# Kernel tuning notes

Measured on AMD Instinct MI355X. Metric: run time of the kernel, lower is better.

## Reference

```python
import jax, jax.numpy as jnp
from jax import lax
import numpy as np

B, S, H, L, NH, DH, DFF, V, NL = 8, 512, 768, 12, 12, 64, 3072, 30522, 19


def _ln(x, s, b):
    m = x.mean(-1, keepdims=True)
    v = ((x - m) ** 2).mean(-1, keepdims=True)
    return (x - m) * lax.rsqrt(v + 1e-12) * s + b


def setup_inputs() -> dict:
    key = jax.random.key(0)
    ks = iter(jax.random.split(key, 40))

    def n(shape, scale=0.02):
        return jax.random.normal(next(ks), shape, jnp.float32) * scale

    return {
        "input_ids": jax.random.randint(next(ks), (B, S), 0, V, jnp.int32),
        "attention_mask": jnp.ones((B, S), jnp.int32),
        "labels": jax.random.randint(next(ks), (B, S), 0, NL, jnp.int32),
        "token_emb": n((V, H)), "pos_emb": n((S, H)),
        "ln_emb_s": jnp.ones((H,)), "ln_emb_b": jnp.zeros((H,)),
        "Wq": n((L, H, H)), "bq": jnp.zeros((L, H)),
        "Wk": n((L, H, H)), "bk": jnp.zeros((L, H)),
        "Wv": n((L, H, H)), "bv": jnp.zeros((L, H)),
        "Wo": n((L, H, H)), "bo": jnp.zeros((L, H)),
        "ln1_s": jnp.ones((L, H)), "ln1_b": jnp.zeros((L, H)),
        "W1": n((L, H, DFF)), "b1": jnp.zeros((L, DFF)),
        "W2": n((L, DFF, H)), "b2": jnp.zeros((L, H)),
        "ln2_s": jnp.ones((L, H)), "ln2_b": jnp.zeros((L, H)),
        "cls_W": n((H, NL)), "cls_b": jnp.zeros((NL,)),
        "start_trans": n((NL,), 0.1), "end_trans": n((NL,), 0.1),
        "trans": n((NL, NL), 0.1),
    }


def reference(input_ids, attention_mask, labels, token_emb, pos_emb, ln_emb_s, ln_emb_b,
              Wq, bq, Wk, bk, Wv, bv, Wo, bo, ln1_s, ln1_b, W1, b1, W2, b2,
              ln2_s, ln2_b, cls_W, cls_b, start_trans, end_trans, trans):
    maskf = attention_mask.astype(jnp.float32)
    # --- BERT encoder (post-LN, eval mode so dropout is identity) ---
    x = token_emb[input_ids] + pos_emb[None, :, :]
    x = _ln(x, ln_emb_s, ln_emb_b)
    bias = (1.0 - maskf)[:, None, None, :] * -1e9  # additive attention mask
    scale = 1.0 / np.sqrt(DH)
    for l in range(L):
        q = (x @ Wq[l] + bq[l]).reshape(B, S, NH, DH)
        k = (x @ Wk[l] + bk[l]).reshape(B, S, NH, DH)
        v = (x @ Wv[l] + bv[l]).reshape(B, S, NH, DH)
        a = jax.nn.softmax(jnp.einsum('bqhd,bkhd->bhqk', q, k) * scale + bias, -1)
        ctx = jnp.einsum('bhqk,bkhd->bqhd', a, v).reshape(B, S, H)
        x = _ln(x + ctx @ Wo[l] + bo[l], ln1_s[l], ln1_b[l])
        h = jax.nn.gelu(x @ W1[l] + b1[l])
        x = _ln(x + h @ W2[l] + b2[l], ln2_s[l], ln2_b[l])
    logits = x @ cls_W + cls_b  # [B, S, NL]
    # --- CRF negative log-likelihood (torchcrf semantics, reduction='sum') ---
    em = jnp.take_along_axis(logits, labels[..., None], -1)[..., 0]  # [B, S]
    num = start_trans[labels[:, 0]] + em[:, 0]
    tr = trans[labels[:, :-1], labels[:, 1:]]  # [B, S-1]
    num = num + jnp.sum((tr + em[:, 1:]) * maskf[:, 1:], -1)
    last_idx = maskf.sum(-1).astype(jnp.int32) - 1
    last_tag = jnp.take_along_axis(labels, last_idx[:, None], 1)[:, 0]
    num = num + end_trans[last_tag]
    # forward algorithm (log-domain DP scan over time)
    alpha0 = start_trans[None, :] + logits[:, 0]  # [B, NL]

    def step(alpha, inp):
        em_t, m_t = inp  # [B, NL], [B]
        nxt = jax.nn.logsumexp(alpha[:, :, None] + trans[None] + em_t[:, None, :], axis=1)
        return jnp.where(m_t[:, None] > 0, nxt, alpha), None

    alpha, _ = lax.scan(step, alpha0,
                        (jnp.swapaxes(logits, 0, 1)[1:], jnp.swapaxes(maskf, 0, 1)[1:]))
    den = jax.nn.logsumexp(alpha + end_trans[None, :], -1)
    return jnp.sum(den - num)  # loss = -sum(llh)
```

## Files before the change

### kernel.cpp

```cpp
#include <hip/hip_runtime.h>
#include <hip/hip_bf16.h>
#include <math.h>

#define B_   8
#define S_   512
#define H_   768
#define L_   12
#define NHD_ 12
#define DH_  64
#define DFF_ 3072
#define NL_  19

#define NCH_ 32
#define CHL_ 16

typedef __bf16 bf16x8 __attribute__((ext_vector_type(8)));
typedef float  f32x4  __attribute__((ext_vector_type(4)));

__device__ __forceinline__ unsigned short f2bf(float f) {
    unsigned int u = __float_as_uint(f);
    u = (u + 0x7fffu + ((u >> 16) & 1u)) >> 16;
    return (unsigned short)u;
}

__device__ __forceinline__ float gelu_f(float x) {
    const float c = 0.7978845608028654f;
    float x3 = x * x * x;
    return 0.5f * x * (1.0f + tanhf(c * (x + 0.044715f * x3)));
}

__device__ __forceinline__ void load_lds16(const unsigned short* g, unsigned short* l) {
    __builtin_amdgcn_global_load_lds(
        (const __attribute__((address_space(1))) unsigned int*)g,
        (__attribute__((address_space(3))) unsigned int*)l,
        16, 0, 0);
}

__global__ __launch_bounds__(256) void prep_layer(
    const float* __restrict__ Wq, const float* __restrict__ Wk,
    const float* __restrict__ Wv, const float* __restrict__ Wo,
    const float* __restrict__ W1, const float* __restrict__ W2,
    const float* __restrict__ bq, const float* __restrict__ bk,
    const float* __restrict__ bv,
    unsigned short* __restrict__ WqkvT, unsigned short* __restrict__ WoT,
    unsigned short* __restrict__ W1T, unsigned short* __restrict__ W2T,
    float* __restrict__ biasc)
{
    __shared__ float t[64][65];
    const int tid = threadIdx.x;
    const int id = blockIdx.x;

    if (id >= 1728) {
        int i = (id - 1728) * 256 + tid;
        if (i < 3 * H_) biasc[i] = (i < H_) ? bq[i] : (i < 2 * H_ ? bk[i - H_] : bv[i - 2 * H_]);
        return;
    }

    const float* src; unsigned short* dst; int K, N, bx, by;
    if (id < 576) {
        int wsel = id / 144, tt = id % 144;
        bx = tt % 12; by = tt / 12; K = H_; N = H_;
        src = (wsel == 0) ? Wq : (wsel == 1) ? Wk : (wsel == 2) ? Wv : Wo;
        dst = (wsel < 3) ? (WqkvT + (size_t)wsel * H_ * H_) : WoT;
    } else if (id < 1152) {
        int tt = id - 576; bx = tt % 48; by = tt / 48; K = H_; N = DFF_; src = W1; dst = W1T;
    } else {
        int tt = id - 1152; bx = tt % 12; by = tt / 12; K = DFF_; N = H_; src = W2; dst = W2T;
    }

    const int n0 = bx * 64, k0 = by * 64;
    #pragma unroll
    for (int p = 0; p < 16; ++p) {
        int idx = p * 256 + tid;
        int i = idx >> 6, j = idx & 63;
        t[i][j] = src[(size_t)(k0 + i) * N + n0 + j];
    }
    __syncthreads();
    #pragma unroll
    for (int p = 0; p < 4; ++p) {
        int q = p * 256 + tid;
        int n = q >> 4, kq = q & 15;
        unsigned int w0 = (unsigned int)f2bf(t[kq * 4 + 0][n]) | ((unsigned int)f2bf(t[kq * 4 + 1][n]) << 16);
        unsigned int w1 = (unsigned int)f2bf(t[kq * 4 + 2][n]) | ((unsigned int)f2bf(t[kq * 4 + 3][n]) << 16);
        uint2 w; w.x = w0; w.y = w1;
        *(uint2*)(dst + (size_t)(n0 + n) * K + k0 + kq * 4) = w;
    }
}

template <int EPI>
__global__ __launch_bounds__(256) void gemm_bf16(
    const unsigned short* __restrict__ A,
    const unsigned short* __restrict__ Bt,
    const float* __restrict__ bias,
    const float* __restrict__ R,
    float* __restrict__ Cf,
    unsigned short* __restrict__ Cb,
    unsigned short* __restrict__ Vt,
    int M, int N, int K)
{
    __shared__ __align__(16) unsigned short As[128 * 32];
    __shared__ __align__(16) unsigned short Bs[128 * 32];
    const int tid  = threadIdx.x;
    const int lane = tid & 63;
    const int wave = tid >> 6;
    const int wm = wave >> 1, wn = wave & 1;
    const int mbase = blockIdx.y * 128;
    const int nbase = blockIdx.x * 128;

    f32x4 acc[4][4];
    #pragma unroll
    for (int mi = 0; mi < 4; ++mi)
        #pragma unroll
        for (int ni = 0; ni < 4; ++ni) acc[mi][ni] = (f32x4){0.f, 0.f, 0.f, 0.f};

    const int crow = tid >> 2;
    const int kc   = tid & 3;
    const unsigned short* ag0 = A  + (size_t)(mbase + crow) * K + kc * 8;
    const unsigned short* ag1 = A  + (size_t)(mbase + 64 + crow) * K + kc * 8;
    const unsigned short* bg0 = Bt + (size_t)(nbase + crow) * K + kc * 8;
    const unsigned short* bg1 = Bt + (size_t)(nbase + 64 + crow) * K + kc * 8;
    unsigned short* la0 = As + (size_t)tid * 8;
    unsigned short* la1 = As + (size_t)(256 + tid) * 8;
    unsigned short* lb0 = Bs + (size_t)tid * 8;
    unsigned short* lb1 = Bs + (size_t)(256 + tid) * 8;

    const int fr = lane & 15;
    const int fc = lane >> 4;

    for (int kk = 0; kk < K; kk += 32) {
        load_lds16(ag0 + kk, la0);
        load_lds16(ag1 + kk, la1);
        load_lds16(bg0 + kk, lb0);
        load_lds16(bg1 + kk, lb1);
        __syncthreads();

        bf16x8 af[4], bf[4];
        #pragma unroll
        for (int mi = 0; mi < 4; ++mi)
            af[mi] = *(const bf16x8*)&As[(size_t)(wm * 64 + mi * 16 + fr) * 32 + fc * 8];
        #pragma unroll
        for (int ni = 0; ni < 4; ++ni)
            bf[ni] = *(const bf16x8*)&Bs[(size_t)(wn * 64 + ni * 16 + fr) * 32 + fc * 8];

        #pragma unroll
        for (int mi = 0; mi < 4; ++mi)
            #pragma unroll
            for (int ni = 0; ni < 4; ++ni)
                acc[mi][ni] = __builtin_amdgcn_mfma_f32_16x16x32_bf16(
                    af[mi], bf[ni], acc[mi][ni], 0, 0, 0);
        __syncthreads();
    }

    const int r0 = (lane >> 4) * 4;
    const int c0 = lane & 15;
    #pragma unroll
    for (int mi = 0; mi < 4; ++mi) {
        const int gm = mbase + wm * 64 + mi * 16 + r0;
        #pragma unroll
        for (int ni = 0; ni < 4; ++ni) {
            const int gn = nbase + wn * 64 + ni * 16 + c0;
            const float bv = bias[gn];
            #pragma unroll
            for (int r = 0; r < 4; ++r) {
                float vv = acc[mi][ni][r] + bv;
                const size_t off = (size_t)(gm + r) * N + gn;
                if (EPI == 1) Cb[off] = f2bf(gelu_f(vv));
                else if (EPI == 2) Cf[off] = vv + R[off];
                else {
                    unsigned short v16 = f2bf(vv);
                    if (gn < 2 * H_) {
                        Cb[off] = v16;
                    } else {
                        int tok = gm + r;
                        Vt[(((size_t)(tok >> 9) * NHD_ + ((gn - 2 * H_) >> 6)) * DH_
                            + (gn & 63)) * S_ + (tok & (S_ - 1))] = v16;
                    }
                }
            }
        }
    }
}

__global__ __launch_bounds__(256) void attn3(
    const unsigned short* __restrict__ qkvb,
    const unsigned short* __restrict__ vtb,
    const int* __restrict__ mask,
    unsigned short* __restrict__ ctxb)
{
    const int qt = blockIdx.x, h = blockIdx.y, b = blockIdx.z;
    const int tid = threadIdx.x;
    const int lane = tid & 63;
    const int w  = tid >> 6;
    const int fr = lane & 15;
    const int fh = lane >> 4;
    const int bh = b * NHD_ + h;

    __shared__ __align__(16) unsigned short Ks[64 * 64];
    __shared__ __align__(16) unsigned short Vts[64 * 64];
    __shared__ __align__(16) unsigned short Ps[4][16][72];
    __shared__ float Ms[64];

    const size_t qrow = (size_t)((b << 9) + (qt << 6) + (w << 4) + fr) * 2304 + (h << 6);
    const bf16x8 qf0 = *(const bf16x8*)&qkvb[qrow + fh * 8];
    const bf16x8 qf1 = *(const bf16x8*)&qkvb[qrow + 32 + fh * 8];

    float m = -1e30f, l = 0.f;
    f32x4 po[4];
    #pragma unroll
    for (int dg = 0; dg < 4; ++dg) po[dg] = (f32x4){0.f, 0.f, 0.f, 0.f};

    const int swz = (fr & 7) << 4;

    for (int kt = 0; kt < 8; ++kt) {
        const int kb = kt << 6;
        __syncthreads();
        {
            int i0 = tid, i1 = tid + 256;
            int r0s = i0 >> 3, r1s = i1 >> 3;
            int c0 = ((i0 & 7) << 4) ^ ((r0s & 7) << 4);
            int c1 = ((i1 & 7) << 4) ^ ((r1s & 7) << 4);
            load_lds16(qkvb + (size_t)((b << 9) + kb + r0s) * 2304 + H_ + (h << 6) + (c0 >> 1), Ks + i0 * 8);
            load_lds16(qkvb + (size_t)((b << 9) + kb + r1s) * 2304 + H_ + (h << 6) + (c1 >> 1), Ks + i1 * 8);
            load_lds16(vtb + ((size_t)(bh << 6) + r0s) * S_ + kb + (c0 >> 1), Vts + i0 * 8);
            load_lds16(vtb + ((size_t)(bh << 6) + r1s) * S_ + kb + (c1 >> 1), Vts + i1 * 8);
        }
        if (tid < 64) Ms[tid] = (1.0f - (float)mask[(b << 9) + kb + tid]) * -1e9f;
        __syncthreads();

        f32x4 sc4[4];
        #pragma unroll
        for (int g = 0; g < 4; ++g) sc4[g] = (f32x4){0.f, 0.f, 0.f, 0.f};
        #pragma unroll
        for (int c = 0; c < 2; ++c) {
            const bf16x8 qf = c ? qf1 : qf0;
            #pragma unroll
            for (int g = 0; g < 4; ++g) {
                bf16x8 kf = *(const bf16x8*)&Ks[((g << 4) + fr) * 64
                              + ((((c << 6) + (fh << 4)) ^ swz) >> 1)];
                sc4[g] = __builtin_amdgcn_mfma_f32_16x16x32_bf16(kf, qf, sc4[g], 0, 0, 0);
            }
        }

        float sv[16];
        float pm = -3e38f;
        #pragma unroll
        for (int g = 0; g < 4; ++g)
            #pragma unroll
            for (int r = 0; r < 4; ++r) {
                float xx = sc4[g][r] * 0.125f + Ms[(g << 4) + (fh << 2) + r];
                sv[g * 4 + r] = xx;
                pm = fmaxf(pm, xx);
            }
        pm = fmaxf(pm, __shfl_xor(pm, 16));
        pm = fmaxf(pm, __shfl_xor(pm, 32));
        const float mnew = fmaxf(m, pm);
        const float alpha = __expf(m - mnew);
        float ps = 0.f;
        #pragma unroll
        for (int i = 0; i < 16; ++i) { sv[i] = __expf(sv[i] - mnew); ps += sv[i]; }
        ps += __shfl_xor(ps, 16);
        ps += __shfl_xor(ps, 32);
        l = l * alpha + ps;
        m = mnew;

        #pragma unroll
        for (int g = 0; g < 4; ++g) {
            unsigned int* pw = (unsigned int*)&Ps[w][fr][(g << 4) + (fh << 2)];
            pw[0] = (unsigned int)f2bf(sv[g * 4 + 0]) | ((unsigned int)f2bf(sv[g * 4 + 1]) << 16);
            pw[1] = (unsigned int)f2bf(sv[g * 4 + 2]) | ((unsigned int)f2bf(sv[g * 4 + 3]) << 16);
        }

        float al[4];
        #pragma unroll
        for (int r = 0; r < 4; ++r) al[r] = __shfl(alpha, (fh << 2) + r);
        #pragma unroll
        for (int dg = 0; dg < 4; ++dg) {
            po[dg][0] *= al[0]; po[dg][1] *= al[1];
            po[dg][2] *= al[2]; po[dg][3] *= al[3];
        }

        const bf16x8 pf0 = *(const bf16x8*)&Ps[w][fr][fh * 8];
        const bf16x8 pf1 = *(const bf16x8*)&Ps[w][fr][32 + fh * 8];
        #pragma unroll
        for (int dg = 0; dg < 4; ++dg) {
            bf16x8 vf0 = *(const bf16x8*)&Vts[((dg << 4) + fr) * 64 + (((fh << 4) ^ swz) >> 1)];
            po[dg] = __builtin_amdgcn_mfma_f32_16x16x32_bf16(pf0, vf0, po[dg], 0, 0, 0);
            bf16x8 vf1 = *(const bf16x8*)&Vts[((dg << 4) + fr) * 64 + (((64 + (fh << 4)) ^ swz) >> 1)];
            po[dg] = __builtin_amdgcn_mfma_f32_16x16x32_bf16(pf1, vf1, po[dg], 0, 0, 0);
        }
    }

    float inv[4];
    #pragma unroll
    for (int r = 0; r < 4; ++r) inv[r] = 1.0f / __shfl(l, (fh << 2) + r);
    #pragma unroll
    for (int r = 0; r < 4; ++r) {
        unsigned short* op = ctxb
            + (size_t)((b << 9) + (qt << 6) + (w << 4) + (fh << 2) + r) * H_
            + (h << 6) + fr;
        #pragma unroll
        for (int dg = 0; dg < 4; ++dg)
            op[dg << 4] = f2bf(po[dg][r] * inv[r]);
    }
}

__global__ __launch_bounds__(256) void ln_kernel(
    const float* __restrict__ in, const float* __restrict__ sc,
    const float* __restrict__ bi, float* __restrict__ out,
    unsigned short* __restrict__ outb)
{
    const int row = blockIdx.x;
    const int tid = threadIdx.x;
    const float* x = in + (size_t)row * H_;
    float v[3], s0 = 0.f, s1 = 0.f;
    #pragma unroll
    for (int r = 0; r < 3; ++r) {
        v[r] = x[tid + r * 256];
        s0 += v[r]; s1 += v[r] * v[r];
    }
    __shared__ float red[8];
    __shared__ float stat[2];
    #pragma unroll
    for (int o = 32; o > 0; o >>= 1) { s0 += __shfl_down(s0, o); s1 += __shfl_down(s1, o); }
    if ((tid & 63) == 0) { red[tid >> 6] = s0; red[4 + (tid >> 6)] = s1; }
    __syncthreads();
    if (tid == 0) {
        float t0 = red[0] + red[1] + red[2] + red[3];
        float t1 = red[4] + red[5] + red[6] + red[7];
        float mean = t0 / H_;
        float var  = t1 / H_ - mean * mean;
        stat[0] = mean;
        stat[1] = rsqrtf(var + 1e-12f);
    }
    __syncthreads();
    float mean = stat[0], rstd = stat[1];
    float* o = out + (size_t)row * H_;
    unsigned short* ob = outb + (size_t)row * H_;
    #pragma unroll
    for (int r = 0; r < 3; ++r) {
        int i = tid + r * 256;
        float rr = (v[r] - mean) * rstd * sc[i] + bi[i];
        o[i] = rr;
        ob[i] = f2bf(rr);
    }
}

__global__ __launch_bounds__(256) void embed_ln_kernel(
    const int* __restrict__ ids, const float* __restrict__ tok,
    const float* __restrict__ pos, const float* __restrict__ sc,
    const float* __restrict__ bi, float* __restrict__ out,
    unsigned short* __restrict__ outb)
{
    const int row = blockIdx.x;
    const int spos = row & (S_ - 1);
    const int tid = threadIdx.x;
    const int id = ids[row];
    const float* t = tok + (size_t)id * H_;
    const float* p = pos + (size_t)spos * H_;
    float v[3], s0 = 0.f, s1 = 0.f;
    #pragma unroll
    for (int r = 0; r < 3; ++r) {
        int i = tid + r * 256;
        v[r] = t[i] + p[i];
        s0 += v[r]; s1 += v[r] * v[r];
    }
    __shared__ float red[8];
    __shared__ float stat[2];
    #pragma unroll
    for (int o = 32; o > 0; o >>= 1) { s0 += __shfl_down(s0, o); s1 += __shfl_down(s1, o); }
    if ((tid & 63) == 0) { red[tid >> 6] = s0; red[4 + (tid >> 6)] = s1; }
    __syncthreads();
    if (tid == 0) {
        float t0 = red[0] + red[1] + red[2] + red[3];
        float t1 = red[4] + red[5] + red[6] + red[7];
        float mean = t0 / H_;
        float var  = t1 / H_ - mean * mean;
        stat[0] = mean;
        stat[1] = rsqrtf(var + 1e-12f);
    }
    __syncthreads();
    float mean = stat[0], rstd = stat[1];
    float* o = out + (size_t)row * H_;
    unsigned short* ob = outb + (size_t)row * H_;
    #pragma unroll
    for (int r = 0; r < 3; ++r) {
        int i = tid + r * 256;
        float rr = (v[r] - mean) * rstd * sc[i] + bi[i];
        o[i] = rr;
        ob[i] = f2bf(rr);
    }
}

__global__ __launch_bounds__(256) void gemm_cls(
    const float* __restrict__ A, const float* __restrict__ W,
    const float* __restrict__ bias, float* __restrict__ C, int M, int N, int K)
{
    __shared__ float As[16][65];
    __shared__ float Ws[16][64];
    const int tid = threadIdx.x;
    const int tx = tid & 15;
    const int ty = tid >> 4;
    const int mbase = blockIdx.y * 64;
    const int nbase = blockIdx.x * 64;
    float acc[4][4] = {};
    for (int kk = 0; kk < K; kk += 16) {
        #pragma unroll
        for (int r = 0; r < 4; ++r) {
            int idx = r * 256 + tid;
            int mm = idx >> 4, k4 = idx & 15;
            As[k4][mm] = A[(size_t)(mbase + mm) * K + kk + k4];
        }
        #pragma unroll
        for (int r = 0; r < 4; ++r) {
            int idx = r * 256 + tid;
            int n = idx & 63, k4 = idx >> 6;
            int gn = nbase + n;
            Ws[k4][n] = (gn < N) ? W[(size_t)(kk + k4) * N + gn] : 0.0f;
        }
        __syncthreads();
        #pragma unroll
        for (int k = 0; k < 16; ++k) {
            float a[4], w[4];
            #pragma unroll
            for (int i = 0; i < 4; ++i) a[i] = As[k][ty * 4 + i];
            #pragma unroll
            for (int j = 0; j < 4; ++j) w[j] = Ws[k][tx * 4 + j];
            #pragma unroll
            for (int i = 0; i < 4; ++i)
                #pragma unroll
                for (int j = 0; j < 4; ++j)
                    acc[i][j] = fmaf(a[i], w[j], acc[i][j]);
        }
        __syncthreads();
    }
    #pragma unroll
    for (int i = 0; i < 4; ++i) {
        int gm = mbase + ty * 4 + i;
        #pragma unroll
        for (int j = 0; j < 4; ++j) {
            int gn = nbase + tx * 4 + j;
            if (gn < N) C[(size_t)gm * N + gn] = acc[i][j] + bias[gn];
        }
    }
}

__global__ __launch_bounds__(256) void crf_num_kernel(
    const float* __restrict__ logits, const int* __restrict__ labels,
    const int* __restrict__ mask, const float* __restrict__ start_trans,
    const float* __restrict__ end_trans, const float* __restrict__ trans,
    float* __restrict__ numb)
{
    const int b = blockIdx.x;
    const int tid = threadIdx.x;
    float lsum = 0.f, lmask = 0.f;
    for (int t = tid; t < S_; t += 256) {
        float mf = (float)mask[b * S_ + t];
        lmask += mf;
        if (t >= 1) {
            int lp = labels[b * S_ + t - 1];
            int lc = labels[b * S_ + t];
            float em = logits[((size_t)b * S_ + t) * NL_ + lc];
            lsum += (trans[lp * NL_ + lc] + em) * mf;
        }
    }
    __shared__ float red[8];
    #pragma unroll
    for (int o = 32; o > 0; o >>= 1) { lsum += __shfl_down(lsum, o); lmask += __shfl_down(lmask, o); }
    if ((tid & 63) == 0) { red[tid >> 6] = lsum; red[4 + (tid >> 6)] = lmask; }
    __syncthreads();
    if (tid == 0) {
        float ts = red[0] + red[1] + red[2] + red[3];
        float tm = red[4] + red[5] + red[6] + red[7];
        int l0 = labels[b * S_];
        float nm = start_trans[l0] + logits[(size_t)b * S_ * NL_ + l0] + ts;
        int last = (int)tm - 1;
        int lt = labels[b * S_ + last];
        nm += end_trans[lt];
        numb[b] = nm;
    }
}

__global__ __launch_bounds__(384) void crf_chunk_kernel(
    const float* __restrict__ logits, const int* __restrict__ mask,
    const float* __restrict__ trans, float* __restrict__ Pg)
{
    const int c = blockIdx.x, b = blockIdx.y;
    const int tid = threadIdx.x;
    const bool act = tid < NL_ * NL_;
    const int i = tid / NL_;
    const int j = tid - i * NL_;

    const int t0 = 1 + c * CHL_;
    const int nt = min(CHL_, S_ - t0);

    __shared__ float P[NL_][20];
    __shared__ float tr_s[NL_ * NL_];
    __shared__ float em_s[CHL_ * NL_];
    __shared__ int mk[CHL_];

    for (int f = tid; f < NL_ * NL_; f += 384) tr_s[f] = trans[f];
    for (int f = tid; f < nt * NL_; f += 384)
        em_s[f] = logits[((size_t)b * S_ + t0) * NL_ + f];
    if (tid < nt) mk[tid] = mask[b * S_ + t0 + tid];
    __syncthreads();

    float trcol[NL_];
    if (act) {
        #pragma unroll
        for (int k = 0; k < NL_; ++k) trcol[k] = tr_s[k * NL_ + j];
        float p0;
        if (mk[0] > 0) p0 = tr_s[i * NL_ + j] + em_s[j];
        else           p0 = (i == j) ? 0.f : -1e30f;
        P[i][j] = p0;
    }
    __syncthreads();

    for (int tt = 1; tt < nt; ++tt) {
        float nv = 0.f;
        if (act) {
            float v[NL_];
            float vmax = -3e38f;
            #pragma unroll
            for (int k = 0; k < NL_; ++k) {
                v[k] = P[i][k] + trcol[k];
                vmax = fmaxf(vmax, v[k]);
            }
            float s = 0.f;
            #pragma unroll
            for (int k = 0; k < NL_; ++k) s += __expf(v[k] - vmax);
            nv = vmax + __logf(s) + em_s[tt * NL_ + j];
        }
        __syncthreads();
        if (act && mk[tt] > 0) P[i][j] = nv;
        __syncthreads();
    }

    if (act) Pg[((size_t)b * NCH_ + c) * (NL_ * NL_) + tid] = P[i][j];
}

__global__ __launch_bounds__(384) void crf_combine_kernel(
    const float* __restrict__ Pg, const float* __restrict__ logits,
    const float* __restrict__ start_trans, const float* __restrict__ end_trans,
    float* __restrict__ denb)
{
    const int b = blockIdx.x;
    const int tid = threadIdx.x;
    __shared__ float Q[NCH_ * NL_ * NL_];
    __shared__ float fin[NL_];

    for (int w = tid; w < NCH_ * NL_ * NL_; w += 384)
        Q[w] = Pg[(size_t)b * NCH_ * NL_ * NL_ + w];
    __syncthreads();

    for (int m = NCH_ / 2; m >= 1; m >>= 1) {
        const int items = m * NL_ * NL_;
        float res[16];
        #pragma unroll
        for (int r = 0; r < 16; ++r) {
            const int w = tid + r * 384;
            if (w < items) {
                const int p = w / (NL_ * NL_);
                const int e = w - p * (NL_ * NL_);
                const int ii = e / NL_;
                const int jj = e - ii * NL_;
                const float* Lm = &Q[(2 * p) * NL_ * NL_ + ii * NL_];
                const float* Rm = &Q[(2 * p + 1) * NL_ * NL_ + jj];
                float v[NL_];
                float vmax = -3e38f;
                #pragma unroll
                for (int k = 0; k < NL_; ++k) {
                    v[k] = Lm[k] + Rm[k * NL_];
                    vmax = fmaxf(vmax, v[k]);
                }
                float s = 0.f;
                #pragma unroll
                for (int k = 0; k < NL_; ++k) s += __expf(v[k] - vmax);
                res[r] = vmax + __logf(s);
            }
        }
        __syncthreads();
        #pragma unroll
        for (int r = 0; r < 16; ++r) {
            const int w = tid + r * 384;
            if (w < items) Q[w] = res[r];
        }
        __syncthreads();
    }

    if (tid < NL_) {
        float v[NL_];
        float vmax = -3e38f;
        #pragma unroll
        for (int k = 0; k < NL_; ++k) {
            v[k] = start_trans[k] + logits[(size_t)b * S_ * NL_ + k] + Q[k * NL_ + tid];
            vmax = fmaxf(vmax, v[k]);
        }
        float s = 0.f;
        #pragma unroll
        for (int k = 0; k < NL_; ++k) s += __expf(v[k] - vmax);
        fin[tid] = vmax + __logf(s) + end_trans[tid];
    }
    __syncthreads();
    if (tid == 0) {
        float vmax = -3e38f;
        #pragma unroll
        for (int k = 0; k < NL_; ++k) vmax = fmaxf(vmax, fin[k]);
        float s = 0.f;
        #pragma unroll
        for (int k = 0; k < NL_; ++k) s += __expf(fin[k] - vmax);
        denb[b] = vmax + __logf(s);
    }
}

__global__ void finalize_kernel(const float* __restrict__ numb,
                                const float* __restrict__ denb,
                                float* __restrict__ out)
{
    if (threadIdx.x == 0 && blockIdx.x == 0) {
        float s = 0.f;
        for (int b = 0; b < B_; ++b) s += denb[b] - numb[b];
        out[0] = s;
    }
}

extern "C" void kernel_launch(void* const* d_in, const int* in_sizes, int n_in,
                              void* d_out, int out_size, void* d_ws, size_t ws_size,
                              hipStream_t stream)
{
    const int*   input_ids = (const int*)d_in[0];
    const int*   attn_mask = (const int*)d_in[1];
    const int*   labels    = (const int*)d_in[2];
    const float* token_emb = (const float*)d_in[3];
    const float* pos_emb   = (const float*)d_in[4];
    const float* ln_emb_s  = (const float*)d_in[5];
    const float* ln_emb_b  = (const float*)d_in[6];
    const float* Wq  = (const float*)d_in[7];
    const float* bq  = (const float*)d_in[8];
    const float* Wk  = (const float*)d_in[9];
    const float* bk  = (const float*)d_in[10];
    const float* Wv  = (const float*)d_in[11];
    const float* bv  = (const float*)d_in[12];
    const float* Wo  = (const float*)d_in[13];
    const float* bo  = (const float*)d_in[14];
    const float* ln1s = (const float*)d_in[15];
    const float* ln1b = (const float*)d_in[16];
    const float* W1  = (const float*)d_in[17];
    const float* b1  = (const float*)d_in[18];
    const float* W2  = (const float*)d_in[19];
    const float* b2  = (const float*)d_in[20];
    const float* ln2s = (const float*)d_in[21];
    const float* ln2b = (const float*)d_in[22];
    const float* cls_W = (const float*)d_in[23];
    const float* cls_b = (const float*)d_in[24];
    const float* start_trans = (const float*)d_in[25];
    const float* end_trans   = (const float*)d_in[26];
    const float* trans       = (const float*)d_in[27];

    char* base = (char*)d_ws;
    const int M = B_ * S_;
    unsigned short* qkvb = (unsigned short*)base;
    unsigned short* vtb  = qkvb + (size_t)M * 2304;
    unsigned short* hbb  = (unsigned short*)base;
    size_t off = (size_t)M * 3072 * 2;
    float*          x     = (float*)(base + off); off += (size_t)M * H_ * 4;
    float*          y     = (float*)(base + off); off += (size_t)M * H_ * 4;
    unsigned short* xb    = (unsigned short*)(base + off); off += (size_t)M * H_ * 2;
    unsigned short* ctxb  = (unsigned short*)(base + off); off += (size_t)M * H_ * 2;
    unsigned short* WqkvT = (unsigned short*)(base + off); off += (size_t)3 * H_ * H_ * 2;
    unsigned short* WoT   = (unsigned short*)(base + off); off += (size_t)H_ * H_ * 2;
    unsigned short* W1T   = (unsigned short*)(base + off); off += (size_t)DFF_ * H_ * 2;
    unsigned short* W2T   = (unsigned short*)(base + off); off += (size_t)H_ * DFF_ * 2;
    float*          biasc = (float*)(base + off); off += 3 * H_ * 4 + 256;
    float*          logits= (float*)(base + off); off += (size_t)M * NL_ * 4;
    float*          numb  = (float*)(base + off); off += 32;
    float*          denb  = (float*)(base + off); off += 32;
    float*          Pg    = (float*)(base + off); off += (size_t)B_ * NCH_ * NL_ * NL_ * 4;

    dim3 blk(256);
    embed_ln_kernel<<<M, blk, 0, stream>>>(input_ids, token_emb, pos_emb, ln_emb_s, ln_emb_b, x, xb);

    for (int l = 0; l < L_; ++l) {
        const size_t oHH = (size_t)l * H_ * H_;
        const size_t oHF = (size_t)l * H_ * DFF_;
        prep_layer<<<1737, blk, 0, stream>>>(
            Wq + oHH, Wk + oHH, Wv + oHH, Wo + oHH, W1 + oHF, W2 + oHF,
            bq + l * H_, bk + l * H_, bv + l * H_,
            WqkvT, WoT, W1T, W2T, biasc);

        gemm_bf16<3><<<dim3(18, 32), blk, 0, stream>>>(xb, WqkvT, biasc, nullptr, nullptr, qkvb, vtb, M, 3 * H_, H_);
        attn3<<<dim3(8, NHD_, B_), blk, 0, stream>>>(qkvb, vtb, attn_mask, ctxb);
        gemm_bf16<2><<<dim3(6, 32), blk, 0, stream>>>(ctxb, WoT, bo + l * H_, x, y, nullptr, nullptr, M, H_, H_);
        ln_kernel<<<M, blk, 0, stream>>>(y, ln1s + l * H_, ln1b + l * H_, x, xb);
        gemm_bf16<1><<<dim3(24, 32), blk, 0, stream>>>(xb, W1T, b1 + l * DFF_, nullptr, nullptr, hbb, nullptr, M, DFF_, H_);
        gemm_bf16<2><<<dim3(6, 32), blk, 0, stream>>>(hbb, W2T, b2 + l * H_, x, y, nullptr, nullptr, M, H_, DFF_);
        ln_kernel<<<M, blk, 0, stream>>>(y, ln2s + l * H_, ln2b + l * H_, x, xb);
    }

    gemm_cls<<<dim3(1, M / 64), blk, 0, stream>>>(x, cls_W, cls_b, logits, M, NL_, H_);
    crf_num_kernel<<<B_, blk, 0, stream>>>(logits, labels, attn_mask, start_trans, end_trans, trans, numb);
    crf_chunk_kernel<<<dim3(NCH_, B_), dim3(384), 0, stream>>>(logits, attn_mask, trans, Pg);
    crf_combine_kernel<<<B_, dim3(384), 0, stream>>>(Pg, logits, start_trans, end_trans, denb);
    finalize_kernel<<<1, 64, 0, stream>>>(numb, denb, (float*)d_out);
}
```

Baseline: 3.161 ms.

## Double-buffer GEMM LDS tiles, swizzle workgroup order, rewrite classifier kernel

After: 2.917 ms. 1.08x faster.

```diff
diff --git a/kernel.cpp b/kernel.cpp
--- a/kernel.cpp
+++ b/kernel.cpp
@@ -98,14 +98,19 @@
     unsigned short* __restrict__ Vt,
     int M, int N, int K)
 {
-    __shared__ __align__(16) unsigned short As[128 * 32];
-    __shared__ __align__(16) unsigned short Bs[128 * 32];
+    __shared__ __align__(16) unsigned short As[2][128 * 32];
+    __shared__ __align__(16) unsigned short Bs[2][128 * 32];
     const int tid  = threadIdx.x;
     const int lane = tid & 63;
     const int wave = tid >> 6;
     const int wm = wave >> 1, wn = wave & 1;
-    const int mbase = blockIdx.y * 128;
-    const int nbase = blockIdx.x * 128;
+
+    const int nwg  = gridDim.x * gridDim.y;
+    const int orig = blockIdx.y * gridDim.x + blockIdx.x;
+    const int cpx  = nwg >> 3;
+    const int sw   = (orig & 7) * cpx + (orig >> 3);
+    const int mbase = (sw / gridDim.x) * 128;
+    const int nbase = (sw % gridDim.x) * 128;
 
     f32x4 acc[4][4];
     #pragma unroll
@@ -119,37 +124,43 @@
     const unsigned short* ag1 = A  + (size_t)(mbase + 64 + crow) * K + kc * 8;
     const unsigned short* bg0 = Bt + (size_t)(nbase + crow) * K + kc * 8;
     const unsigned short* bg1 = Bt + (size_t)(nbase + 64 + crow) * K + kc * 8;
-    unsigned short* la0 = As + (size_t)tid * 8;
-    unsigned short* la1 = As + (size_t)(256 + tid) * 8;
-    unsigned short* lb0 = Bs + (size_t)tid * 8;
-    unsigned short* lb1 = Bs + (size_t)(256 + tid) * 8;
 
     const int fr = lane & 15;
     const int fc = lane >> 4;
 
+#define STAGE_(c, kk) do { \
+        load_lds16(ag0 + (kk), As[c] + (size_t)tid * 8); \
+        load_lds16(ag1 + (kk), As[c] + (size_t)(256 + tid) * 8); \
+        load_lds16(bg0 + (kk), Bs[c] + (size_t)tid * 8); \
+        load_lds16(bg1 + (kk), Bs[c] + (size_t)(256 + tid) * 8); \
+    } while (0)
+
+    STAGE_(0, 0);
+    __syncthreads();
+
+    int cur = 0;
     for (int kk = 0; kk < K; kk += 32) {
-        load_lds16(ag0 + kk, la0);
-        load_lds16(ag1 + kk, la1);
-        load_lds16(bg0 + kk, lb0);
-        load_lds16(bg1 + kk, lb1);
-        __syncthreads();
-
-        bf16x8 af[4], bf[4];
+        if (kk + 32 < K) STAGE_(cur ^ 1, kk + 32);
+
+        bf16x8 af[4], bf4[4];
         #pragma unroll
         for (int mi = 0; mi < 4; ++mi)
-            af[mi] = *(const bf16x8*)&As[(size_t)(wm * 64 + mi * 16 + fr) * 32 + fc * 8];
+            af[mi] = *(const bf16x8*)&As[cur][(size_t)(wm * 64 + mi * 16 + fr) * 32 + fc * 8];
         #pragma unroll
         for (int ni = 0; ni < 4; ++ni)
-            bf[ni] = *(const bf16x8*)&Bs[(size_t)(wn * 64 + ni * 16 + fr) * 32 + fc * 8];
+            bf4[ni] = *(const bf16x8*)&Bs[cur][(size_t)(wn * 64 + ni * 16 + fr) * 32 + fc * 8];
 
         #pragma unroll
         for (int mi = 0; mi < 4; ++mi)
             #pragma unroll
             for (int ni = 0; ni < 4; ++ni)
                 acc[mi][ni] = __builtin_amdgcn_mfma_f32_16x16x32_bf16(
-                    af[mi], bf[ni], acc[mi][ni], 0, 0, 0);
+                    af[mi], bf4[ni], acc[mi][ni], 0, 0, 0);
+
         __syncthreads();
-    }
+        cur ^= 1;
+    }
+#undef STAGE_
 
     const int r0 = (lane >> 4) * 4;
     const int c0 = lane & 15;
@@ -393,55 +404,28 @@
 
 __global__ __launch_bounds__(256) void gemm_cls(
     const float* __restrict__ A, const float* __restrict__ W,
-    const float* __restrict__ bias, float* __restrict__ C, int M, int N, int K)
-{
-    __shared__ float As[16][65];
-    __shared__ float Ws[16][64];
-    const int tid = threadIdx.x;
-    const int tx = tid & 15;
-    const int ty = tid >> 4;
-    const int mbase = blockIdx.y * 64;
-    const int nbase = blockIdx.x * 64;
-    float acc[4][4] = {};
-    for (int kk = 0; kk < K; kk += 16) {
-        #pragma unroll
-        for (int r = 0; r < 4; ++r) {
-            int idx = r * 256 + tid;
-            int mm = idx >> 4, k4 = idx & 15;
-            As[k4][mm] = A[(size_t)(mbase + mm) * K + kk + k4];
-        }
-        #pragma unroll
-        for (int r = 0; r < 4; ++r) {
-            int idx = r * 256 + tid;
-            int n = idx & 63, k4 = idx >> 6;
-            int gn = nbase + n;
-            Ws[k4][n] = (gn < N) ? W[(size_t)(kk + k4) * N + gn] : 0.0f;
-        }
-        __syncthreads();
-        #pragma unroll
-        for (int k = 0; k < 16; ++k) {
-            float a[4], w[4];
-            #pragma unroll
-            for (int i = 0; i < 4; ++i) a[i] = As[k][ty * 4 + i];
-            #pragma unroll
-            for (int j = 0; j < 4; ++j) w[j] = Ws[k][tx * 4 + j];
-            #pragma unroll
-            for (int i = 0; i < 4; ++i)
-                #pragma unroll
-                for (int j = 0; j < 4; ++j)
-                    acc[i][j] = fmaf(a[i], w[j], acc[i][j]);
-        }
-        __syncthreads();
-    }
-    #pragma unroll
-    for (int i = 0; i < 4; ++i) {
-        int gm = mbase + ty * 4 + i;
-        #pragma unroll
-        for (int j = 0; j < 4; ++j) {
-            int gn = nbase + tx * 4 + j;
-            if (gn < N) C[(size_t)gm * N + gn] = acc[i][j] + bias[gn];
-        }
-    }
+    const float* __restrict__ bias, float* __restrict__ C)
+{
+    __shared__ float Ws[H_ * NL_];
+    const int tid = threadIdx.x;
+    for (int i = tid; i < H_ * NL_; i += 256) Ws[i] = W[i];
+    __syncthreads();
+
+    const int g   = blockIdx.x * 256 + tid;
+    const int row = g >> 5;
+    const int col = g & 31;
+    if (col >= NL_) return;
+
+    const float* a = A + (size_t)row * H_;
+    float acc = 0.f;
+    for (int k = 0; k < H_; k += 4) {
+        f32x4 a4 = *(const f32x4*)(a + k);
+        acc = fmaf(a4[0], Ws[(k + 0) * NL_ + col],
+              fmaf(a4[1], Ws[(k + 1) * NL_ + col],
+              fmaf(a4[2], Ws[(k + 2) * NL_ + col],
+              fmaf(a4[3], Ws[(k + 3) * NL_ + col], acc))));
+    }
+    C[(size_t)row * NL_ + col] = acc + bias[col];
 }
 
 __global__ __launch_bounds__(256) void crf_num_kernel(
@@ -696,7 +680,7 @@
         ln_kernel<<<M, blk, 0, stream>>>(y, ln2s + l * H_, ln2b + l * H_, x, xb);
     }
 
-    gemm_cls<<<dim3(1, M / 64), blk, 0, stream>>>(x, cls_W, cls_b, logits, M, NL_, H_);
+    gemm_cls<<<dim3(M * 32 / 256), blk, 0, stream>>>(x, cls_W, cls_b, logits);
     crf_num_kernel<<<B_, blk, 0, stream>>>(logits, labels, attn_mask, start_trans, end_trans, trans, numb);
     crf_chunk_kernel<<<dim3(NCH_, B_), dim3(384), 0, stream>>>(logits, attn_mask, trans, Pg);
     crf_combine_kernel<<<B_, dim3(384), 0, stream>>>(Pg, logits, start_trans, end_trans, denb);
```
